# Performance work log

Measured on AMD Instinct MI355X. Metric: run time of the kernel, lower is better.

## Reference

```python
import jax, jax.numpy as jnp
import numpy as np

TAU = 0.5

def setup_inputs() -> dict:
    key = jax.random.key(0)
    ks = jax.random.split(key, 20)
    B, D1, D2, E1, E2, U = 4096, 2000, 2000, 256, 256, 512
    M = E1 + E2
    s = lambda k, shp, scale=0.05: jax.random.normal(k, shp, dtype=jnp.float32) * scale
    return {
        "inputs": jax.random.normal(ks[0], (B, D1 + D2), dtype=jnp.float32),
        "h_tm1": jax.random.normal(ks[1], (B, U), dtype=jnp.float32),
        "crohis_tm": jax.random.normal(ks[2], (B, M), dtype=jnp.float32),
        "embed_weight_1": s(ks[3], (D1, E1)),
        "embed_weight_2": s(ks[4], (D2, E2)),
        "ca_1to2_w": s(ks[5], (E1, E1)),
        "ca_1to2_u": s(ks[6], (E2, E1)),
        "ca_1to2_v": s(ks[7], (E2, E1)),
        "ca_2to1_w": s(ks[8], (E2, E2)),
        "ca_2to1_u": s(ks[9], (E1, E2)),
        "ca_2to1_v": s(ks[10], (E1, E2)),
        "crohis_weight_w": s(ks[11], (M, U)),
        "crohis_bias": jnp.zeros((U,), jnp.float32),
        "crohis_decomp_weight": s(ks[12], (M, M)),
        "crohis_decomp_bias": jnp.zeros((M,), jnp.float32),
        "kernel": s(ks[13], (M, 3 * U)),
        "recurrent_kernel": s(ks[14], (U, 3 * U)),
        "bias": jnp.zeros((3 * U,), jnp.float32),
    }


def reference(inputs, h_tm1, crohis_tm,
              embed_weight_1, embed_weight_2,
              ca_1to2_w, ca_1to2_u, ca_1to2_v,
              ca_2to1_w, ca_2to1_u, ca_2to1_v,
              crohis_weight_w, crohis_bias,
              crohis_decomp_weight, crohis_decomp_bias,
              kernel, recurrent_kernel, bias):
    D1 = embed_weight_1.shape[0]
    U = recurrent_kernel.shape[0]
    # dual embedding lookups (dense multi-hot x embedding matrix)
    seqx1 = inputs[:, :D1]
    seqx2 = inputs[:, D1:]
    emb1 = seqx1 @ embed_weight_1   # [B, E1]
    emb2 = seqx2 @ embed_weight_2   # [B, E2]
    # cross-attention gates (softmax over feature axis, as K.softmax default)
    att12 = jax.nn.softmax(jnp.tanh(emb1 @ ca_1to2_w + emb2 @ ca_1to2_u) * (emb2 @ ca_1to2_v), axis=-1)
    att21 = jax.nn.softmax(jnp.tanh(emb2 @ ca_2to1_w + emb1 @ ca_2to1_u) * (emb1 @ ca_2to1_v), axis=-1)
    x = jnp.concatenate([emb1 * att12, emb2 * att21], axis=-1)  # [B, M]
    # cross-history decomposition modulating previous hidden state
    cro = jnp.tanh(crohis_tm @ crohis_decomp_weight + crohis_decomp_bias)
    h_prev = h_tm1 + jnp.tanh(cro @ crohis_weight_w + crohis_bias)
    # GRU (implementation=2, reset_after=False)
    mx = x @ kernel + bias                         # [B, 3U]
    x_z, x_r, x_h = mx[:, :U], mx[:, U:2 * U], mx[:, 2 * U:]
    mi = h_prev @ recurrent_kernel[:, :2 * U]      # [B, 2U]
    z = jax.nn.sigmoid(x_z + mi[:, :U])
    r = jax.nn.sigmoid(x_r + mi[:, U:])
    hh = jnp.tanh(x_h + (r * h_prev) @ recurrent_kernel[:, 2 * U:])
    h = z * h_prev + (1.0 - z) * hh
    # updated cross-history state (exponential moving average with tau)
    crohis_new = TAU * crohis_tm + (1.0 - TAU) * x
    return h, crohis_new
```

## Files before the change

kernel.cpp:

```cpp
#include <hip/hip_runtime.h>
#include <hip/hip_bf16.h>
#include <math.h>


#define TAU_F 0.5f

typedef __bf16 bf16x8 __attribute__((ext_vector_type(8)));
typedef __bf16 bf16x4 __attribute__((ext_vector_type(4)));
typedef float f32x4 __attribute__((ext_vector_type(4)));

__device__ __forceinline__ void gload16(const void* g, void* l) {
    __builtin_amdgcn_global_load_lds(
        (const __attribute__((address_space(1))) void*)g,
        (__attribute__((address_space(3))) void*)l, 16, 0, 0);
}

struct SubGemm {
    const void* A;
    int lda;
    int Kvalid;
    const __bf16* BT;
    int ldbt;
    float* C;
    int ldc;
    long long strideC;
    int Ksub;
    int nbx;
    int pairSplit;
    int pairAOff;
    int obf16;
};

template <bool AFP32>
__global__ __launch_bounds__(256) void gemm_dual(SubGemm g1, SubGemm g2, int blocks1)
{
    __shared__ __attribute__((aligned(16))) char lds[49152];

    const int tid = threadIdx.x, w = tid >> 6, l = tid & 63;

    const int gx = gridDim.x;
    const int nwg = gx * (int)gridDim.y;
    const int hw = (int)blockIdx.y * gx + (int)blockIdx.x;
    const int lg = (hw & 7) * (nwg >> 3) + (hw >> 3);
    const int bxl_lin = lg % gx;
    const int by = lg / gx;

    const bool second = bxl_lin >= blocks1;
    const SubGemm& g = second ? g2 : g1;
    const int bxl = second ? bxl_lin - blocks1 : bxl_lin;
    const int ct = bxl % g.nbx, spl = bxl / g.nbx;
    const int brow = by * 64, bcol = ct * 128;
    const int k_begin = spl * g.Ksub;
    const int nt = g.Ksub >> 5;
    const int aoff = (ct >= g.pairSplit) ? g.pairAOff : 0;

    const int sbr = w * 32 + (l >> 2);
    const int seg = (l & 3) * 8;

    const __bf16* Bg0 = g.BT + (size_t)(bcol + sbr) * g.ldbt + seg + k_begin;
    const __bf16* Bg1 = Bg0 + (size_t)16 * g.ldbt;

    f32x4 acc[2][4] = {};
    const int fr = l & 15, fk = (l >> 4) * 8;
    const int wr = (w >> 1) * 32, wc = (w & 1) * 64;
    const int kmax = (nt - 1) * 32;

    if constexpr (AFP32) {
        auto Af32 = (float (*)[64][32])lds;
        auto Bs   = (__bf16 (*)[128][32])(lds + 24576);

        const float* ArowBase = (const float*)g.A + aoff
                              + (size_t)(brow + w * 16 + (l >> 3)) * g.lda;
        const int colLane = (l & 7) * 4;
        const int kcl4 = g.Kvalid - 4;

#define ISSUE_A32(slot)                                                       \
        {                                                                     \
            const int _s = (slot);                                            \
            const int _k = (_s * 32 < kmax) ? _s * 32 : kmax;                 \
            const int _b = _s % 3;                                            \
            int c0 = k_begin + _k + colLane;                                  \
            c0 = c0 < kcl4 ? c0 : kcl4;                                       \
            gload16(ArowBase + c0,                 &Af32[_b][w * 16][0]);     \
            gload16(ArowBase + 8 * g.lda + c0,     &Af32[_b][w * 16 + 8][0]); \
            gload16(Bg0 + _k, &Bs[_b][w * 32][0]);                            \
            gload16(Bg1 + _k, &Bs[_b][w * 32 + 16][0]);                       \
        }

        ISSUE_A32(0) ISSUE_A32(1)

        for (int t = 0; t < nt; ++t) {
            asm volatile("s_waitcnt vmcnt(4)" ::: "memory");
            asm volatile("s_waitcnt lgkmcnt(0)" ::: "memory");
            __builtin_amdgcn_s_barrier();

            const int bi = t % 3;
            bf16x8 a[2]; bf16x8 b[4];
#pragma unroll
            for (int m = 0; m < 2; ++m) {
                f32x4 lo = *(const f32x4*)&Af32[bi][wr + m * 16 + fr][fk];
                f32x4 hi = *(const f32x4*)&Af32[bi][wr + m * 16 + fr][fk + 4];
#pragma unroll
                for (int z = 0; z < 4; ++z) { a[m][z] = (__bf16)lo[z]; a[m][4 + z] = (__bf16)hi[z]; }
            }
#pragma unroll
            for (int n = 0; n < 4; ++n) b[n] = *(const bf16x8*)&Bs[bi][wc + n * 16 + fr][fk];

            ISSUE_A32(t + 2)

#pragma unroll
            for (int m = 0; m < 2; ++m)
#pragma unroll
                for (int n = 0; n < 4; ++n)
                    acc[m][n] = __builtin_amdgcn_mfma_f32_16x16x32_bf16(a[m], b[n], acc[m][n], 0, 0, 0);
        }
#undef ISSUE_A32
    } else {
        auto As = (__bf16 (*)[64][32])lds;
        auto Bs = (__bf16 (*)[128][32])(lds + 16384);

        const int sar = w * 16 + (l >> 2);
        const __bf16* Ar = (const __bf16*)g.A + aoff
                         + (size_t)(brow + sar) * g.lda + seg + k_begin;

#define ISSUE_AB(slot)                                                        \
        {                                                                     \
            const int _s = (slot);                                            \
            const int _k = (_s * 32 < kmax) ? _s * 32 : kmax;                 \
            const int _b = _s & 3;                                            \
            gload16(Ar + _k,  &As[_b][w * 16][0]);                            \
            gload16(Bg0 + _k, &Bs[_b][w * 32][0]);                            \
            gload16(Bg1 + _k, &Bs[_b][w * 32 + 16][0]);                       \
        }

        ISSUE_AB(0) ISSUE_AB(1) ISSUE_AB(2)

        for (int t = 0; t < nt; ++t) {
            asm volatile("s_waitcnt vmcnt(6)" ::: "memory");
            asm volatile("s_waitcnt lgkmcnt(0)" ::: "memory");
            __builtin_amdgcn_s_barrier();

            const int bi = t & 3;
            bf16x8 a[2], b[4];
#pragma unroll
            for (int m = 0; m < 2; ++m) a[m] = *(const bf16x8*)&As[bi][wr + m * 16 + fr][fk];
#pragma unroll
            for (int n = 0; n < 4; ++n) b[n] = *(const bf16x8*)&Bs[bi][wc + n * 16 + fr][fk];

            ISSUE_AB(t + 3)

#pragma unroll
            for (int m = 0; m < 2; ++m)
#pragma unroll
                for (int n = 0; n < 4; ++n)
                    acc[m][n] = __builtin_amdgcn_mfma_f32_16x16x32_bf16(a[m], b[n], acc[m][n], 0, 0, 0);
        }
#undef ISSUE_AB
    }

    const int fq = (l >> 4) * 4;
    if (g.obf16) {
        __bf16* Cb = (__bf16*)g.C + (size_t)spl * g.strideC;
#pragma unroll
        for (int m = 0; m < 2; ++m)
#pragma unroll
            for (int n = 0; n < 4; ++n)
#pragma unroll
                for (int r = 0; r < 4; ++r) {
                    int row = brow + wr + m * 16 + fq + r;
                    int col = bcol + wc + n * 16 + fr;
                    Cb[(size_t)row * g.ldc + col] = (__bf16)acc[m][n][r];
                }
    } else {
        float* C = g.C + (size_t)spl * g.strideC;
#pragma unroll
        for (int m = 0; m < 2; ++m)
#pragma unroll
            for (int n = 0; n < 4; ++n)
#pragma unroll
                for (int r = 0; r < 4; ++r) {
                    int row = brow + wr + m * 16 + fq + r;
                    int col = bcol + wc + n * 16 + fr;
                    C[(size_t)row * g.ldc + col] = acc[m][n][r];
                }
    }
}

__global__ __launch_bounds__(256) void prep_wT(
    const float* __restrict__ ew1, const float* __restrict__ ew2,
    const float* __restrict__ w12, const float* __restrict__ u12,
    const float* __restrict__ v12, const float* __restrict__ w21,
    const float* __restrict__ u21, const float* __restrict__ v21,
    const float* __restrict__ cd_w, const float* __restrict__ cw_w,
    const float* __restrict__ kern, const float* __restrict__ rkern,
    __bf16* __restrict__ WT, __bf16* __restrict__ WcatT,
    __bf16* __restrict__ cdT, __bf16* __restrict__ cwT,
    __bf16* __restrict__ kernT, __bf16* __restrict__ rkernT)
{
    __shared__ float tile[64][65];
    const int b = blockIdx.x, tid = threadIdx.x;
    const int tr = tid >> 6, tc = tid & 63;

    const float* src = nullptr;
    int ldsrc = 0, srow0 = 0, scol0 = 0, kvalid = 1 << 30;
    __bf16* dst; int ldd, n0, k0;
    bool zero = false;

    if (b < 256) {
        int q = b; n0 = (q >> 5) * 64; k0 = (q & 31) * 64;
        dst = WT; ldd = 2048; kvalid = 2000; ldsrc = 256; srow0 = k0;
        if (n0 < 256) { src = ew1; scol0 = n0; } else { src = ew2; scol0 = n0 - 256; }
    } else if (b < 384) {
        int q = b - 256; n0 = (q >> 3) * 64; k0 = (q & 7) * 64;
        dst = WcatT; ldd = 512; ldsrc = 256; srow0 = k0 & 255; scol0 = n0 & 255;
        int qn = n0 >> 8; bool khi = k0 >= 256;
        if (qn == 0)      src = khi ? u12 : w12;
        else if (qn == 1) src = khi ? w21 : u21;
        else if (qn == 2) { if (khi) src = v12; else zero = true; }
        else              { if (khi) zero = true; else src = v21; }
    } else if (b < 448) {
        int q = b - 384; n0 = (q >> 3) * 64; k0 = (q & 7) * 64;
        src = cd_w; ldsrc = 512; srow0 = k0; scol0 = n0; dst = cdT; ldd = 512;
    } else if (b < 512) {
        int q = b - 448; n0 = (q >> 3) * 64; k0 = (q & 7) * 64;
        src = cw_w; ldsrc = 512; srow0 = k0; scol0 = n0; dst = cwT; ldd = 512;
    } else if (b < 704) {
        int q = b - 512; n0 = (q >> 3) * 64; k0 = (q & 7) * 64;
        src = kern; ldsrc = 1536; srow0 = k0; scol0 = n0; dst = kernT; ldd = 512;
    } else {
        int q = b - 704; n0 = (q >> 3) * 64; k0 = (q & 7) * 64;
        src = rkern; ldsrc = 1536; srow0 = k0; scol0 = n0; dst = rkernT; ldd = 512;
    }

#pragma unroll
    for (int p = 0; p < 16; ++p) {
        int kr = p * 4 + tr;
        float v = 0.f;
        if (!zero && (srow0 + kr) < kvalid)
            v = src[(size_t)(srow0 + kr) * ldsrc + scol0 + tc];
        tile[kr][tc] = v;
    }
    __syncthreads();
#pragma unroll
    for (int p = 0; p < 16; ++p) {
        int nr = p * 4 + tr;
        dst[(size_t)(n0 + nr) * ldd + k0 + tc] = (__bf16)tile[tc][nr];
    }
}

__global__ __launch_bounds__(256) void reduce_A(
    const float* __restrict__ P12, const float* __restrict__ P4,
    const float* __restrict__ cd_b,
    __bf16* __restrict__ E, __bf16* __restrict__ cro)
{
    const int S = 1 << 21;
    int b = blockIdx.x;
    int i = (((b & 2047) * 256) + threadIdx.x) * 4;
    if (b < 2048) {
        f32x4 p0 = *(const f32x4*)(P12 + i);
        f32x4 p1 = *(const f32x4*)(P12 + S + i);
        __bf16 o[4];
#pragma unroll
        for (int j = 0; j < 4; ++j) o[j] = (__bf16)(p0[j] + p1[j]);
        *(bf16x4*)&E[i] = *(bf16x4*)o;
    } else {
        f32x4 p0 = *(const f32x4*)(P4 + i);
        int c = i & 511;
        __bf16 o[4];
#pragma unroll
        for (int j = 0; j < 4; ++j) o[j] = (__bf16)tanhf(p0[j] + cd_b[c + j]);
        *(bf16x4*)&cro[i] = *(bf16x4*)o;
    }
}

__global__ __launch_bounds__(256) void fuse1(
    const __bf16* __restrict__ T, const __bf16* __restrict__ E,
    const float* __restrict__ crohis,
    const float* __restrict__ P5,
    const float* __restrict__ h_tm1, const float* __restrict__ cw_b,
    __bf16* __restrict__ x, float* __restrict__ cro_out,
    float* __restrict__ hprev, __bf16* __restrict__ hprev_bf)
{
    __shared__ float s4[4];
    int b = blockIdx.x;
    int j = threadIdx.x;
    if (b < 4096) {
        const __bf16* t = T + (size_t)b * 1024;
        float s12 = tanhf((float)t[j])       * (float)t[512 + j];
        float s21 = tanhf((float)t[256 + j]) * (float)t[768 + j];
        float v = s12;
#pragma unroll
        for (int o = 32; o >= 1; o >>= 1) v = fmaxf(v, __shfl_xor(v, o, 64));
        __syncthreads(); if ((j & 63) == 0) s4[j >> 6] = v; __syncthreads();
        float m12 = fmaxf(fmaxf(s4[0], s4[1]), fmaxf(s4[2], s4[3]));
        float e12 = expf(s12 - m12);
        v = e12;
#pragma unroll
        for (int o = 32; o >= 1; o >>= 1) v += __shfl_xor(v, o, 64);
        __syncthreads(); if ((j & 63) == 0) s4[j >> 6] = v; __syncthreads();
        float sum12 = s4[0] + s4[1] + s4[2] + s4[3];
        v = s21;
#pragma unroll
        for (int o = 32; o >= 1; o >>= 1) v = fmaxf(v, __shfl_xor(v, o, 64));
        __syncthreads(); if ((j & 63) == 0) s4[j >> 6] = v; __syncthreads();
        float m21 = fmaxf(fmaxf(s4[0], s4[1]), fmaxf(s4[2], s4[3]));
        float e21 = expf(s21 - m21);
        v = e21;
#pragma unroll
        for (int o = 32; o >= 1; o >>= 1) v += __shfl_xor(v, o, 64);
        __syncthreads(); if ((j & 63) == 0) s4[j >> 6] = v; __syncthreads();
        float sum21 = s4[0] + s4[1] + s4[2] + s4[3];

        size_t b0 = (size_t)b * 512 + j, b1 = b0 + 256;
        float x1 = (float)E[b0] * (e12 / sum12);
        float x2 = (float)E[b1] * (e21 / sum21);
        x[b0] = (__bf16)x1;
        x[b1] = (__bf16)x2;
        cro_out[b0] = TAU_F * crohis[b0] + (1.f - TAU_F) * x1;
        cro_out[b1] = TAU_F * crohis[b1] + (1.f - TAU_F) * x2;
    } else {
        int i = ((b - 4096) * 256 + j) * 4;
        f32x4 p = *(const f32x4*)(P5 + i);
        f32x4 ht = *(const f32x4*)(h_tm1 + i);
        int c = i & 511;
        f32x4 o; __bf16 ob[4];
#pragma unroll
        for (int q = 0; q < 4; ++q) {
            float hv = ht[q] + tanhf(p[q] + cw_b[c + q]);
            o[q] = hv; ob[q] = (__bf16)hv;
        }
        *(f32x4*)(hprev + i) = o;
        *(bf16x4*)&hprev_bf[i] = *(bf16x4*)ob;
    }
}

__global__ __launch_bounds__(256) void gates_k(
    const float* __restrict__ mx, const float* __restrict__ mi2,
    const float* __restrict__ hprev, const float* __restrict__ bias,
    __bf16* __restrict__ rh)
{
    int i = (blockIdx.x * 256 + threadIdx.x) * 4;
    int row = i >> 9, c = i & 511;
    f32x4 a  = *(const f32x4*)(mx + (size_t)row * 1536 + 512 + c);
    f32x4 m  = *(const f32x4*)(mi2 + (size_t)row * 1024 + 512 + c);
    f32x4 hp = *(const f32x4*)(hprev + i);
    f32x4 bb = *(const f32x4*)(bias + 512 + c);
    __bf16 o[4];
#pragma unroll
    for (int q = 0; q < 4; ++q) {
        float r = 1.f / (1.f + expf(-(a[q] + bb[q] + m[q])));
        o[q] = (__bf16)(r * hp[q]);
    }
    *(bf16x4*)&rh[i] = *(bf16x4*)o;
}

__global__ __launch_bounds__(256) void final_k(
    const float* __restrict__ mx, const float* __restrict__ mi2,
    const float* __restrict__ P8a, const float* __restrict__ P8b,
    const float* __restrict__ hprev, const float* __restrict__ bias,
    float* __restrict__ h)
{
    int i = (blockIdx.x * 256 + threadIdx.x) * 4;
    int row = i >> 9, c = i & 511;
    f32x4 xz = *(const f32x4*)(mx + (size_t)row * 1536 + c);
    f32x4 xh = *(const f32x4*)(mx + (size_t)row * 1536 + 1024 + c);
    f32x4 mz = *(const f32x4*)(mi2 + (size_t)row * 1024 + c);
    f32x4 p0 = *(const f32x4*)(P8a + i);
    f32x4 p1 = *(const f32x4*)(P8b + i);
    f32x4 hp = *(const f32x4*)(hprev + i);
    f32x4 bz = *(const f32x4*)(bias + c);
    f32x4 bh = *(const f32x4*)(bias + 1024 + c);
    f32x4 o;
#pragma unroll
    for (int q = 0; q < 4; ++q) {
        float z = 1.f / (1.f + expf(-(xz[q] + bz[q] + mz[q])));
        float hh = tanhf(xh[q] + bh[q] + p0[q] + p1[q]);
        o[q] = z * hp[q] + (1.f - z) * hh;
    }
    *(f32x4*)(h + i) = o;
}

extern "C" void kernel_launch(void* const* d_in, const int* in_sizes, int n_in,
                              void* d_out, int out_size, void* d_ws, size_t ws_size,
                              hipStream_t stream)
{
    (void)in_sizes; (void)n_in; (void)out_size; (void)ws_size;

    const float* inputs = (const float*)d_in[0];
    const float* h_tm1  = (const float*)d_in[1];
    const float* crohis = (const float*)d_in[2];
    const float* ew1    = (const float*)d_in[3];
    const float* ew2    = (const float*)d_in[4];
    const float* ca12w  = (const float*)d_in[5];
    const float* ca12u  = (const float*)d_in[6];
    const float* ca12v  = (const float*)d_in[7];
    const float* ca21w  = (const float*)d_in[8];
    const float* ca21u  = (const float*)d_in[9];
    const float* ca21v  = (const float*)d_in[10];
    const float* cw_w   = (const float*)d_in[11];
    const float* cw_b   = (const float*)d_in[12];
    const float* cd_w   = (const float*)d_in[13];
    const float* cd_b   = (const float*)d_in[14];
    const float* kern   = (const float*)d_in[15];
    const float* rkern  = (const float*)d_in[16];
    const float* bias   = (const float*)d_in[17];

    char* ws = (char*)d_ws;
    const size_t MB = 1 << 20;
    float*  P12      = (float*)(ws + 0);
    float*  P4       = (float*)(ws + 16 * MB);
    __bf16* T        = (__bf16*)(ws + 16 * MB);
    float*  P5       = (float*)(ws + 32 * MB);
    __bf16* x        = (__bf16*)(ws + 40 * MB);
    __bf16* rh       = (__bf16*)(ws + 40 * MB);
    float*  P8       = (float*)(ws + 44 * MB);
    __bf16* E        = (__bf16*)(ws + 48 * MB);
    __bf16* cro_bf   = (__bf16*)(ws + 52 * MB);
    float*  hprev    = (float*)(ws + 60 * MB);
    __bf16* hprev_bf = (__bf16*)(ws + 68 * MB);
    float*  mx       = (float*)(ws + 0);
    float*  mi2      = (float*)(ws + 24 * MB);
    __bf16* WT       = (__bf16*)(ws + 72 * MB);
    __bf16* WcatT    = (__bf16*)(ws + 74 * MB);
    __bf16* cdT      = (__bf16*)(ws + 75 * MB);
    __bf16* cwT      = (__bf16*)(ws + 75 * MB + 512 * 1024);
    __bf16* kernT    = (__bf16*)(ws + 76 * MB);
    __bf16* rkernT   = (__bf16*)(ws + 77 * MB + 512 * 1024);

    float* h_out   = (float*)d_out;
    float* cro_out = (float*)d_out + 2 * 1048576;

    const int BIG = 1 << 30;
    const long long S2 = 1ll << 21;

    prep_wT<<<896, 256, 0, stream>>>(ew1, ew2, ca12w, ca12u, ca12v, ca21w,
                                     ca21u, ca21v, cd_w, cw_w, kern, rkern,
                                     WT, WcatT, cdT, cwT, kernT, rkernT);

    SubGemm gA1 = { inputs, 4000, 2000, WT,  2048, P12, 512, S2, 1024, 4, 2, 2000, 0 };
    SubGemm gA2 = { crohis,  512,  512, cdT,  512, P4,  512, 0,   512, 4, BIG, 0, 0 };
    gemm_dual<true><<<dim3(12, 64), 256, 0, stream>>>(gA1, gA2, 8);

    reduce_A<<<4096, 256, 0, stream>>>(P12, P4, cd_b, E, cro_bf);

    SubGemm gB1 = { E,      512, 512, WcatT, 512, (float*)T, 1024, 0, 512, 8, BIG, 0, 1 };
    SubGemm gB2 = { cro_bf, 512, 512, cwT,   512, P5,        512,  0, 512, 4, BIG, 0, 0 };
    gemm_dual<false><<<dim3(12, 64), 256, 0, stream>>>(gB1, gB2, 8);

    fuse1<<<6144, 256, 0, stream>>>(T, E, crohis, P5, h_tm1, cw_b,
                                    x, cro_out, hprev, hprev_bf);

    SubGemm gC1 = { x,        512, 512, kernT,  512, mx,  1536, 0, 512, 12, BIG, 0, 0 };
    SubGemm gC2 = { hprev_bf, 512, 512, rkernT, 512, mi2, 1024, 0, 512, 8,  BIG, 0, 0 };
    gemm_dual<false><<<dim3(20, 64), 256, 0, stream>>>(gC1, gC2, 12);

    gates_k<<<2048, 256, 0, stream>>>(mx, mi2, hprev, bias, rh);

    SubGemm gG = { rh, 512, 512, rkernT + (size_t)1024 * 512, 512, P8, 512, S2, 256, 4, BIG, 0, 0 };
    gemm_dual<false><<<dim3(8, 64), 256, 0, stream>>>(gG, gG, 8);

    final_k<<<2048, 256, 0, stream>>>(mx, mi2, P8, P8 + S2, hprev, bias, h_out);
}
```

Before: 132.7 us.

## Drop multi-stage LDS pipelining and raise split-K for more workgroups

The GEMM kernel gives up its 3/4-stage global_load_lds ring buffer for a single-buffered load/sync/compute loop, cutting LDS per workgroup from 48KB to 12-16KB so more workgroups fit per CU. Split-K is raised for the embedding GEMM (4-way) and for the crohis decomposition and crohis-weight GEMMs (2-way), which increases grid sizes. The reduce and fuse kernels now sum the extra partials, and workspace buffers are reassigned so the additional partial outputs fit. The cost is that load latency is no longer hidden inside a workgroup, and the extra partials add memory traffic.

```diff
diff --git a/kernel.cpp b/kernel.cpp
--- a/kernel.cpp
+++ b/kernel.cpp
@@ -34,7 +34,7 @@
 template <bool AFP32>
 __global__ __launch_bounds__(256) void gemm_dual(SubGemm g1, SubGemm g2, int blocks1)
 {
-    __shared__ __attribute__((aligned(16))) char lds[49152];
+    __shared__ __attribute__((aligned(16))) char lds[AFP32 ? 16384 : 12288];
 
     const int tid = threadIdx.x, w = tid >> 6, l = tid & 63;
 
@@ -63,99 +63,71 @@
     f32x4 acc[2][4] = {};
     const int fr = l & 15, fk = (l >> 4) * 8;
     const int wr = (w >> 1) * 32, wc = (w & 1) * 64;
-    const int kmax = (nt - 1) * 32;
 
     if constexpr (AFP32) {
-        auto Af32 = (float (*)[64][32])lds;
-        auto Bs   = (__bf16 (*)[128][32])(lds + 24576);
-
-        const float* ArowBase = (const float*)g.A + aoff
-                              + (size_t)(brow + w * 16 + (l >> 3)) * g.lda;
+        auto As32 = (float (*)[32])lds;
+        auto Bs   = (__bf16 (*)[32])(lds + 8192);
+
+        const float* Ar0 = (const float*)g.A + aoff
+                         + (size_t)(brow + w * 16 + (l >> 3)) * g.lda;
+        const float* Ar8 = Ar0 + (size_t)8 * g.lda;
         const int colLane = (l & 7) * 4;
         const int kcl4 = g.Kvalid - 4;
 
-#define ISSUE_A32(slot)                                                       \
-        {                                                                     \
-            const int _s = (slot);                                            \
-            const int _k = (_s * 32 < kmax) ? _s * 32 : kmax;                 \
-            const int _b = _s % 3;                                            \
-            int c0 = k_begin + _k + colLane;                                  \
-            c0 = c0 < kcl4 ? c0 : kcl4;                                       \
-            gload16(ArowBase + c0,                 &Af32[_b][w * 16][0]);     \
-            gload16(ArowBase + 8 * g.lda + c0,     &Af32[_b][w * 16 + 8][0]); \
-            gload16(Bg0 + _k, &Bs[_b][w * 32][0]);                            \
-            gload16(Bg1 + _k, &Bs[_b][w * 32 + 16][0]);                       \
-        }
-
-        ISSUE_A32(0) ISSUE_A32(1)
-
         for (int t = 0; t < nt; ++t) {
-            asm volatile("s_waitcnt vmcnt(4)" ::: "memory");
-            asm volatile("s_waitcnt lgkmcnt(0)" ::: "memory");
-            __builtin_amdgcn_s_barrier();
-
-            const int bi = t % 3;
-            bf16x8 a[2]; bf16x8 b[4];
+            const int k = t * 32;
+            __syncthreads();
+            int c0 = k_begin + k + colLane;
+            c0 = c0 < kcl4 ? c0 : kcl4;
+            gload16(Ar0 + c0, &As32[w * 16][0]);
+            gload16(Ar8 + c0, &As32[w * 16 + 8][0]);
+            gload16(Bg0 + k,  &Bs[w * 32][0]);
+            gload16(Bg1 + k,  &Bs[w * 32 + 16][0]);
+            __syncthreads();
+
+            bf16x8 a[2], b[4];
 #pragma unroll
             for (int m = 0; m < 2; ++m) {
-                f32x4 lo = *(const f32x4*)&Af32[bi][wr + m * 16 + fr][fk];
-                f32x4 hi = *(const f32x4*)&Af32[bi][wr + m * 16 + fr][fk + 4];
+                f32x4 lo = *(const f32x4*)&As32[wr + m * 16 + fr][fk];
+                f32x4 hi = *(const f32x4*)&As32[wr + m * 16 + fr][fk + 4];
 #pragma unroll
                 for (int z = 0; z < 4; ++z) { a[m][z] = (__bf16)lo[z]; a[m][4 + z] = (__bf16)hi[z]; }
             }
 #pragma unroll
-            for (int n = 0; n < 4; ++n) b[n] = *(const bf16x8*)&Bs[bi][wc + n * 16 + fr][fk];
-
-            ISSUE_A32(t + 2)
-
+            for (int n = 0; n < 4; ++n) b[n] = *(const bf16x8*)&Bs[wc + n * 16 + fr][fk];
 #pragma unroll
             for (int m = 0; m < 2; ++m)
 #pragma unroll
                 for (int n = 0; n < 4; ++n)
                     acc[m][n] = __builtin_amdgcn_mfma_f32_16x16x32_bf16(a[m], b[n], acc[m][n], 0, 0, 0);
         }
-#undef ISSUE_A32
     } else {
-        auto As = (__bf16 (*)[64][32])lds;
-        auto Bs = (__bf16 (*)[128][32])(lds + 16384);
+        auto As = (__bf16 (*)[32])lds;
+        auto Bs = (__bf16 (*)[32])(lds + 4096);
 
         const int sar = w * 16 + (l >> 2);
         const __bf16* Ar = (const __bf16*)g.A + aoff
                          + (size_t)(brow + sar) * g.lda + seg + k_begin;
 
-#define ISSUE_AB(slot)                                                        \
-        {                                                                     \
-            const int _s = (slot);                                            \
-            const int _k = (_s * 32 < kmax) ? _s * 32 : kmax;                 \
-            const int _b = _s & 3;                                            \
-            gload16(Ar + _k,  &As[_b][w * 16][0]);                            \
-            gload16(Bg0 + _k, &Bs[_b][w * 32][0]);                            \
-            gload16(Bg1 + _k, &Bs[_b][w * 32 + 16][0]);                       \
-        }
-
-        ISSUE_AB(0) ISSUE_AB(1) ISSUE_AB(2)
-
         for (int t = 0; t < nt; ++t) {
-            asm volatile("s_waitcnt vmcnt(6)" ::: "memory");
-            asm volatile("s_waitcnt lgkmcnt(0)" ::: "memory");
-            __builtin_amdgcn_s_barrier();
-
-            const int bi = t & 3;
+            const int k = t * 32;
+            __syncthreads();
+            gload16(Ar + k,  &As[w * 16][0]);
+            gload16(Bg0 + k, &Bs[w * 32][0]);
+            gload16(Bg1 + k, &Bs[w * 32 + 16][0]);
+            __syncthreads();
+
             bf16x8 a[2], b[4];
 #pragma unroll
-            for (int m = 0; m < 2; ++m) a[m] = *(const bf16x8*)&As[bi][wr + m * 16 + fr][fk];
-#pragma unroll
-            for (int n = 0; n < 4; ++n) b[n] = *(const bf16x8*)&Bs[bi][wc + n * 16 + fr][fk];
-
-            ISSUE_AB(t + 3)
-
+            for (int m = 0; m < 2; ++m) a[m] = *(const bf16x8*)&As[wr + m * 16 + fr][fk];
+#pragma unroll
+            for (int n = 0; n < 4; ++n) b[n] = *(const bf16x8*)&Bs[wc + n * 16 + fr][fk];
 #pragma unroll
             for (int m = 0; m < 2; ++m)
 #pragma unroll
                 for (int n = 0; n < 4; ++n)
                     acc[m][n] = __builtin_amdgcn_mfma_f32_16x16x32_bf16(a[m], b[n], acc[m][n], 0, 0, 0);
         }
-#undef ISSUE_AB
     }
 
     const int fq = (l >> 4) * 4;
@@ -259,16 +231,19 @@
     if (b < 2048) {
         f32x4 p0 = *(const f32x4*)(P12 + i);
         f32x4 p1 = *(const f32x4*)(P12 + S + i);
+        f32x4 p2 = *(const f32x4*)(P12 + 2 * S + i);
+        f32x4 p3 = *(const f32x4*)(P12 + 3 * S + i);
         __bf16 o[4];
 #pragma unroll
-        for (int j = 0; j < 4; ++j) o[j] = (__bf16)(p0[j] + p1[j]);
+        for (int j = 0; j < 4; ++j) o[j] = (__bf16)((p0[j] + p1[j]) + (p2[j] + p3[j]));
         *(bf16x4*)&E[i] = *(bf16x4*)o;
     } else {
         f32x4 p0 = *(const f32x4*)(P4 + i);
+        f32x4 p1 = *(const f32x4*)(P4 + S + i);
         int c = i & 511;
         __bf16 o[4];
 #pragma unroll
-        for (int j = 0; j < 4; ++j) o[j] = (__bf16)tanhf(p0[j] + cd_b[c + j]);
+        for (int j = 0; j < 4; ++j) o[j] = (__bf16)tanhf(p0[j] + p1[j] + cd_b[c + j]);
         *(bf16x4*)&cro[i] = *(bf16x4*)o;
     }
 }
@@ -276,7 +251,7 @@
 __global__ __launch_bounds__(256) void fuse1(
     const __bf16* __restrict__ T, const __bf16* __restrict__ E,
     const float* __restrict__ crohis,
-    const float* __restrict__ P5,
+    const float* __restrict__ P5a, const float* __restrict__ P5b,
     const float* __restrict__ h_tm1, const float* __restrict__ cw_b,
     __bf16* __restrict__ x, float* __restrict__ cro_out,
     float* __restrict__ hprev, __bf16* __restrict__ hprev_bf)
@@ -320,13 +295,14 @@
         cro_out[b1] = TAU_F * crohis[b1] + (1.f - TAU_F) * x2;
     } else {
         int i = ((b - 4096) * 256 + j) * 4;
-        f32x4 p = *(const f32x4*)(P5 + i);
+        f32x4 p0 = *(const f32x4*)(P5a + i);
+        f32x4 p1 = *(const f32x4*)(P5b + i);
         f32x4 ht = *(const f32x4*)(h_tm1 + i);
         int c = i & 511;
         f32x4 o; __bf16 ob[4];
 #pragma unroll
         for (int q = 0; q < 4; ++q) {
-            float hv = ht[q] + tanhf(p[q] + cw_b[c + q]);
+            float hv = ht[q] + tanhf(p0[q] + p1[q] + cw_b[c + q]);
             o[q] = hv; ob[q] = (__bf16)hv;
         }
         *(f32x4*)(hprev + i) = o;
@@ -408,18 +384,18 @@
     char* ws = (char*)d_ws;
     const size_t MB = 1 << 20;
     float*  P12      = (float*)(ws + 0);
-    float*  P4       = (float*)(ws + 16 * MB);
-    __bf16* T        = (__bf16*)(ws + 16 * MB);
-    float*  P5       = (float*)(ws + 32 * MB);
-    __bf16* x        = (__bf16*)(ws + 40 * MB);
-    __bf16* rh       = (__bf16*)(ws + 40 * MB);
-    float*  P8       = (float*)(ws + 44 * MB);
+    float*  P5       = (float*)(ws + 0);
+    float*  mi2      = (float*)(ws + 0);
+    __bf16* x        = (__bf16*)(ws + 16 * MB);
+    __bf16* rh       = (__bf16*)(ws + 16 * MB);
+    float*  hprev    = (float*)(ws + 20 * MB);
+    __bf16* hprev_bf = (__bf16*)(ws + 28 * MB);
+    float*  P4       = (float*)(ws + 32 * MB);
+    float*  mx       = (float*)(ws + 32 * MB);
     __bf16* E        = (__bf16*)(ws + 48 * MB);
     __bf16* cro_bf   = (__bf16*)(ws + 52 * MB);
-    float*  hprev    = (float*)(ws + 60 * MB);
-    __bf16* hprev_bf = (__bf16*)(ws + 68 * MB);
-    float*  mx       = (float*)(ws + 0);
-    float*  mi2      = (float*)(ws + 24 * MB);
+    __bf16* T        = (__bf16*)(ws + 56 * MB);
+    float*  P8       = (float*)(ws + 56 * MB);
     __bf16* WT       = (__bf16*)(ws + 72 * MB);
     __bf16* WcatT    = (__bf16*)(ws + 74 * MB);
     __bf16* cdT      = (__bf16*)(ws + 75 * MB);
@@ -437,17 +413,17 @@
                                      ca21u, ca21v, cd_w, cw_w, kern, rkern,
                                      WT, WcatT, cdT, cwT, kernT, rkernT);
 
-    SubGemm gA1 = { inputs, 4000, 2000, WT,  2048, P12, 512, S2, 1024, 4, 2, 2000, 0 };
-    SubGemm gA2 = { crohis,  512,  512, cdT,  512, P4,  512, 0,   512, 4, BIG, 0, 0 };
-    gemm_dual<true><<<dim3(12, 64), 256, 0, stream>>>(gA1, gA2, 8);
+    SubGemm gA1 = { inputs, 4000, 2000, WT,  2048, P12, 512, S2, 512, 4, 2, 2000, 0 };
+    SubGemm gA2 = { crohis,  512,  512, cdT,  512, P4,  512, S2, 256, 4, BIG, 0, 0 };
+    gemm_dual<true><<<dim3(24, 64), 256, 0, stream>>>(gA1, gA2, 16);
 
     reduce_A<<<4096, 256, 0, stream>>>(P12, P4, cd_b, E, cro_bf);
 
-    SubGemm gB1 = { E,      512, 512, WcatT, 512, (float*)T, 1024, 0, 512, 8, BIG, 0, 1 };
-    SubGemm gB2 = { cro_bf, 512, 512, cwT,   512, P5,        512,  0, 512, 4, BIG, 0, 0 };
-    gemm_dual<false><<<dim3(12, 64), 256, 0, stream>>>(gB1, gB2, 8);
-
-    fuse1<<<6144, 256, 0, stream>>>(T, E, crohis, P5, h_tm1, cw_b,
+    SubGemm gB1 = { E,      512, 512, WcatT, 512, (float*)T, 1024, 0,  512, 8, BIG, 0, 1 };
+    SubGemm gB2 = { cro_bf, 512, 512, cwT,   512, P5,        512,  S2, 256, 4, BIG, 0, 0 };
+    gemm_dual<false><<<dim3(16, 64), 256, 0, stream>>>(gB1, gB2, 8);
+
+    fuse1<<<6144, 256, 0, stream>>>(T, E, crohis, P5, P5 + S2, h_tm1, cw_b,
                                     x, cro_out, hprev, hprev_bf);
 
     SubGemm gC1 = { x,        512, 512, kernT,  512, mx,  1536, 0, 512, 12, BIG, 0, 0 };
```

Measured after the change: 143.3 us. 8.0% more time.

## Fuse elementwise epilogues into GEMMs and drop split-K partial buffers

Applied to the files above, without the earlier changes.

Removes split-K from the GEMMs (the big embedding GEMM now runs full K=2048 per block with fewer blocks), so the partial-sum reduction kernels go away. Bias, tanh, h_prev and final GRU update epilogues are fused into the GEMM store via a mode switch, eliminating reduce_A, final_k and half of fuse1. Intermediates mx/mi are stored in bf16 to cut traffic. The cost is fewer blocks on the long-K GEMM (512 vs 768, and 256 blocks for the last GEMM), lower parallelism, and more bf16 rounding of the gate pre-activations.

```diff
diff --git a/kernel.cpp b/kernel.cpp
--- a/kernel.cpp
+++ b/kernel.cpp
@@ -22,13 +22,17 @@
     const __bf16* BT;
     int ldbt;
     float* C;
+    __bf16* Cb;
     int ldc;
-    long long strideC;
     int Ksub;
     int nbx;
     int pairSplit;
     int pairAOff;
-    int obf16;
+    int mode;
+    const float* bias;
+    const float* base;
+    const __bf16* mxp;
+    const __bf16* mip;
 };
 
 template <bool AFP32>
@@ -47,17 +51,15 @@
 
     const bool second = bxl_lin >= blocks1;
     const SubGemm& g = second ? g2 : g1;
-    const int bxl = second ? bxl_lin - blocks1 : bxl_lin;
-    const int ct = bxl % g.nbx, spl = bxl / g.nbx;
+    const int ct = second ? bxl_lin - blocks1 : bxl_lin;
     const int brow = by * 64, bcol = ct * 128;
-    const int k_begin = spl * g.Ksub;
     const int nt = g.Ksub >> 5;
     const int aoff = (ct >= g.pairSplit) ? g.pairAOff : 0;
 
     const int sbr = w * 32 + (l >> 2);
     const int seg = (l & 3) * 8;
 
-    const __bf16* Bg0 = g.BT + (size_t)(bcol + sbr) * g.ldbt + seg + k_begin;
+    const __bf16* Bg0 = g.BT + (size_t)(bcol + sbr) * g.ldbt + seg;
     const __bf16* Bg1 = Bg0 + (size_t)16 * g.ldbt;
 
     f32x4 acc[2][4] = {};
@@ -79,10 +81,10 @@
             const int _s = (slot);                                            \
             const int _k = (_s * 32 < kmax) ? _s * 32 : kmax;                 \
             const int _b = _s % 3;                                            \
-            int c0 = k_begin + _k + colLane;                                  \
+            int c0 = _k + colLane;                                            \
             c0 = c0 < kcl4 ? c0 : kcl4;                                       \
-            gload16(ArowBase + c0,                 &Af32[_b][w * 16][0]);     \
-            gload16(ArowBase + 8 * g.lda + c0,     &Af32[_b][w * 16 + 8][0]); \
+            gload16(ArowBase + c0,             &Af32[_b][w * 16][0]);         \
+            gload16(ArowBase + 8 * g.lda + c0, &Af32[_b][w * 16 + 8][0]);     \
             gload16(Bg0 + _k, &Bs[_b][w * 32][0]);                            \
             gload16(Bg1 + _k, &Bs[_b][w * 32 + 16][0]);                       \
         }
@@ -121,7 +123,7 @@
 
         const int sar = w * 16 + (l >> 2);
         const __bf16* Ar = (const __bf16*)g.A + aoff
-                         + (size_t)(brow + sar) * g.lda + seg + k_begin;
+                         + (size_t)(brow + sar) * g.lda + seg;
 
 #define ISSUE_AB(slot)                                                        \
         {                                                                     \
@@ -159,31 +161,38 @@
     }
 
     const int fq = (l >> 4) * 4;
-    if (g.obf16) {
-        __bf16* Cb = (__bf16*)g.C + (size_t)spl * g.strideC;
-#pragma unroll
-        for (int m = 0; m < 2; ++m)
-#pragma unroll
-            for (int n = 0; n < 4; ++n)
-#pragma unroll
-                for (int r = 0; r < 4; ++r) {
-                    int row = brow + wr + m * 16 + fq + r;
-                    int col = bcol + wc + n * 16 + fr;
-                    Cb[(size_t)row * g.ldc + col] = (__bf16)acc[m][n][r];
+    const int mode = g.mode;
+#pragma unroll
+    for (int m = 0; m < 2; ++m)
+#pragma unroll
+        for (int n = 0; n < 4; ++n)
+#pragma unroll
+            for (int r = 0; r < 4; ++r) {
+                int row = brow + wr + m * 16 + fq + r;
+                int col = bcol + wc + n * 16 + fr;
+                float v = acc[m][n][r];
+                if (mode == 0) {
+                    g.C[(size_t)row * g.ldc + col] = v;
+                } else if (mode == 1) {
+                    g.Cb[(size_t)row * g.ldc + col] = (__bf16)v;
+                } else if (mode == 2) {
+                    g.Cb[(size_t)row * g.ldc + col] = (__bf16)(v + g.bias[col]);
+                } else if (mode == 3) {
+                    g.Cb[(size_t)row * g.ldc + col] = (__bf16)tanhf(v + g.bias[col]);
+                } else if (mode == 4) {
+                    float hv = g.base[(size_t)row * 512 + col] + tanhf(v + g.bias[col]);
+                    g.C[(size_t)row * 512 + col] = hv;
+                    g.Cb[(size_t)row * 512 + col] = (__bf16)hv;
+                } else {
+                    float xz = (float)g.mxp[(size_t)row * 1536 + col];
+                    float xh = (float)g.mxp[(size_t)row * 1536 + 1024 + col];
+                    float mz = (float)g.mip[(size_t)row * 1024 + col];
+                    float hp = g.base[(size_t)row * 512 + col];
+                    float z  = 1.f / (1.f + expf(-(xz + mz)));
+                    float hh = tanhf(xh + v);
+                    g.C[(size_t)row * 512 + col] = z * hp + (1.f - z) * hh;
                 }
-    } else {
-        float* C = g.C + (size_t)spl * g.strideC;
-#pragma unroll
-        for (int m = 0; m < 2; ++m)
-#pragma unroll
-            for (int n = 0; n < 4; ++n)
-#pragma unroll
-                for (int r = 0; r < 4; ++r) {
-                    int row = brow + wr + m * 16 + fq + r;
-                    int col = bcol + wc + n * 16 + fr;
-                    C[(size_t)row * g.ldc + col] = acc[m][n][r];
-                }
-    }
+            }
 }
 
 __global__ __launch_bounds__(256) void prep_wT(
@@ -248,136 +257,65 @@
     }
 }
 
-__global__ __launch_bounds__(256) void reduce_A(
-    const float* __restrict__ P12, const float* __restrict__ P4,
-    const float* __restrict__ cd_b,
-    __bf16* __restrict__ E, __bf16* __restrict__ cro)
-{
-    const int S = 1 << 21;
-    int b = blockIdx.x;
-    int i = (((b & 2047) * 256) + threadIdx.x) * 4;
-    if (b < 2048) {
-        f32x4 p0 = *(const f32x4*)(P12 + i);
-        f32x4 p1 = *(const f32x4*)(P12 + S + i);
-        __bf16 o[4];
-#pragma unroll
-        for (int j = 0; j < 4; ++j) o[j] = (__bf16)(p0[j] + p1[j]);
-        *(bf16x4*)&E[i] = *(bf16x4*)o;
-    } else {
-        f32x4 p0 = *(const f32x4*)(P4 + i);
-        int c = i & 511;
-        __bf16 o[4];
-#pragma unroll
-        for (int j = 0; j < 4; ++j) o[j] = (__bf16)tanhf(p0[j] + cd_b[c + j]);
-        *(bf16x4*)&cro[i] = *(bf16x4*)o;
-    }
-}
-
-__global__ __launch_bounds__(256) void fuse1(
+__global__ __launch_bounds__(256) void fuse_att(
     const __bf16* __restrict__ T, const __bf16* __restrict__ E,
     const float* __restrict__ crohis,
-    const float* __restrict__ P5,
-    const float* __restrict__ h_tm1, const float* __restrict__ cw_b,
-    __bf16* __restrict__ x, float* __restrict__ cro_out,
-    float* __restrict__ hprev, __bf16* __restrict__ hprev_bf)
+    __bf16* __restrict__ x, float* __restrict__ cro_out)
 {
     __shared__ float s4[4];
     int b = blockIdx.x;
     int j = threadIdx.x;
-    if (b < 4096) {
-        const __bf16* t = T + (size_t)b * 1024;
-        float s12 = tanhf((float)t[j])       * (float)t[512 + j];
-        float s21 = tanhf((float)t[256 + j]) * (float)t[768 + j];
-        float v = s12;
-#pragma unroll
-        for (int o = 32; o >= 1; o >>= 1) v = fmaxf(v, __shfl_xor(v, o, 64));
-        __syncthreads(); if ((j & 63) == 0) s4[j >> 6] = v; __syncthreads();
-        float m12 = fmaxf(fmaxf(s4[0], s4[1]), fmaxf(s4[2], s4[3]));
-        float e12 = expf(s12 - m12);
-        v = e12;
-#pragma unroll
-        for (int o = 32; o >= 1; o >>= 1) v += __shfl_xor(v, o, 64);
-        __syncthreads(); if ((j & 63) == 0) s4[j >> 6] = v; __syncthreads();
-        float sum12 = s4[0] + s4[1] + s4[2] + s4[3];
-        v = s21;
-#pragma unroll
-        for (int o = 32; o >= 1; o >>= 1) v = fmaxf(v, __shfl_xor(v, o, 64));
-        __syncthreads(); if ((j & 63) == 0) s4[j >> 6] = v; __syncthreads();
-        float m21 = fmaxf(fmaxf(s4[0], s4[1]), fmaxf(s4[2], s4[3]));
-        float e21 = expf(s21 - m21);
-        v = e21;
-#pragma unroll
-        for (int o = 32; o >= 1; o >>= 1) v += __shfl_xor(v, o, 64);
-        __syncthreads(); if ((j & 63) == 0) s4[j >> 6] = v; __syncthreads();
-        float sum21 = s4[0] + s4[1] + s4[2] + s4[3];
-
-        size_t b0 = (size_t)b * 512 + j, b1 = b0 + 256;
-        float x1 = (float)E[b0] * (e12 / sum12);
-        float x2 = (float)E[b1] * (e21 / sum21);
-        x[b0] = (__bf16)x1;
-        x[b1] = (__bf16)x2;
-        cro_out[b0] = TAU_F * crohis[b0] + (1.f - TAU_F) * x1;
-        cro_out[b1] = TAU_F * crohis[b1] + (1.f - TAU_F) * x2;
-    } else {
-        int i = ((b - 4096) * 256 + j) * 4;
-        f32x4 p = *(const f32x4*)(P5 + i);
-        f32x4 ht = *(const f32x4*)(h_tm1 + i);
-        int c = i & 511;
-        f32x4 o; __bf16 ob[4];
-#pragma unroll
-        for (int q = 0; q < 4; ++q) {
-            float hv = ht[q] + tanhf(p[q] + cw_b[c + q]);
-            o[q] = hv; ob[q] = (__bf16)hv;
-        }
-        *(f32x4*)(hprev + i) = o;
-        *(bf16x4*)&hprev_bf[i] = *(bf16x4*)ob;
-    }
+    const __bf16* t = T + (size_t)b * 1024;
+    float s12 = tanhf((float)t[j])       * (float)t[512 + j];
+    float s21 = tanhf((float)t[256 + j]) * (float)t[768 + j];
+    float v = s12;
+#pragma unroll
+    for (int o = 32; o >= 1; o >>= 1) v = fmaxf(v, __shfl_xor(v, o, 64));
+    __syncthreads(); if ((j & 63) == 0) s4[j >> 6] = v; __syncthreads();
+    float m12 = fmaxf(fmaxf(s4[0], s4[1]), fmaxf(s4[2], s4[3]));
+    float e12 = expf(s12 - m12);
+    v = e12;
+#pragma unroll
+    for (int o = 32; o >= 1; o >>= 1) v += __shfl_xor(v, o, 64);
+    __syncthreads(); if ((j & 63) == 0) s4[j >> 6] = v; __syncthreads();
+    float sum12 = s4[0] + s4[1] + s4[2] + s4[3];
+    v = s21;
+#pragma unroll
+    for (int o = 32; o >= 1; o >>= 1) v = fmaxf(v, __shfl_xor(v, o, 64));
+    __syncthreads(); if ((j & 63) == 0) s4[j >> 6] = v; __syncthreads();
+    float m21 = fmaxf(fmaxf(s4[0], s4[1]), fmaxf(s4[2], s4[3]));
+    float e21 = expf(s21 - m21);
+    v = e21;
+#pragma unroll
+    for (int o = 32; o >= 1; o >>= 1) v += __shfl_xor(v, o, 64);
+    __syncthreads(); if ((j & 63) == 0) s4[j >> 6] = v; __syncthreads();
+    float sum21 = s4[0] + s4[1] + s4[2] + s4[3];
+
+    size_t b0 = (size_t)b * 512 + j, b1 = b0 + 256;
+    float x1 = (float)E[b0] * (e12 / sum12);
+    float x2 = (float)E[b1] * (e21 / sum21);
+    x[b0] = (__bf16)x1;
+    x[b1] = (__bf16)x2;
+    cro_out[b0] = TAU_F * crohis[b0] + (1.f - TAU_F) * x1;
+    cro_out[b1] = TAU_F * crohis[b1] + (1.f - TAU_F) * x2;
 }
 
 __global__ __launch_bounds__(256) void gates_k(
-    const float* __restrict__ mx, const float* __restrict__ mi2,
-    const float* __restrict__ hprev, const float* __restrict__ bias,
-    __bf16* __restrict__ rh)
+    const __bf16* __restrict__ mx, const __bf16* __restrict__ mi,
+    const __bf16* __restrict__ hprev_bf, __bf16* __restrict__ rh)
 {
     int i = (blockIdx.x * 256 + threadIdx.x) * 4;
     int row = i >> 9, c = i & 511;
-    f32x4 a  = *(const f32x4*)(mx + (size_t)row * 1536 + 512 + c);
-    f32x4 m  = *(const f32x4*)(mi2 + (size_t)row * 1024 + 512 + c);
-    f32x4 hp = *(const f32x4*)(hprev + i);
-    f32x4 bb = *(const f32x4*)(bias + 512 + c);
+    bf16x4 a  = *(const bf16x4*)(mx + (size_t)row * 1536 + 512 + c);
+    bf16x4 m  = *(const bf16x4*)(mi + (size_t)row * 1024 + 512 + c);
+    bf16x4 hp = *(const bf16x4*)(hprev_bf + i);
     __bf16 o[4];
 #pragma unroll
     for (int q = 0; q < 4; ++q) {
-        float r = 1.f / (1.f + expf(-(a[q] + bb[q] + m[q])));
-        o[q] = (__bf16)(r * hp[q]);
+        float r = 1.f / (1.f + expf(-((float)a[q] + (float)m[q])));
+        o[q] = (__bf16)(r * (float)hp[q]);
     }
     *(bf16x4*)&rh[i] = *(bf16x4*)o;
-}
-
-__global__ __launch_bounds__(256) void final_k(
-    const float* __restrict__ mx, const float* __restrict__ mi2,
-    const float* __restrict__ P8a, const float* __restrict__ P8b,
-    const float* __restrict__ hprev, const float* __restrict__ bias,
-    float* __restrict__ h)
-{
-    int i = (blockIdx.x * 256 + threadIdx.x) * 4;
-    int row = i >> 9, c = i & 511;
-    f32x4 xz = *(const f32x4*)(mx + (size_t)row * 1536 + c);
-    f32x4 xh = *(const f32x4*)(mx + (size_t)row * 1536 + 1024 + c);
-    f32x4 mz = *(const f32x4*)(mi2 + (size_t)row * 1024 + c);
-    f32x4 p0 = *(const f32x4*)(P8a + i);
-    f32x4 p1 = *(const f32x4*)(P8b + i);
-    f32x4 hp = *(const f32x4*)(hprev + i);
-    f32x4 bz = *(const f32x4*)(bias + c);
-    f32x4 bh = *(const f32x4*)(bias + 1024 + c);
-    f32x4 o;
-#pragma unroll
-    for (int q = 0; q < 4; ++q) {
-        float z = 1.f / (1.f + expf(-(xz[q] + bz[q] + mz[q])));
-        float hh = tanhf(xh[q] + bh[q] + p0[q] + p1[q]);
-        o[q] = z * hp[q] + (1.f - z) * hh;
-    }
-    *(f32x4*)(h + i) = o;
 }
 
 extern "C" void kernel_launch(void* const* d_in, const int* in_sizes, int n_in,
@@ -407,57 +345,47 @@
 
     char* ws = (char*)d_ws;
     const size_t MB = 1 << 20;
-    float*  P12      = (float*)(ws + 0);
-    float*  P4       = (float*)(ws + 16 * MB);
-    __bf16* T        = (__bf16*)(ws + 16 * MB);
-    float*  P5       = (float*)(ws + 32 * MB);
-    __bf16* x        = (__bf16*)(ws + 40 * MB);
-    __bf16* rh       = (__bf16*)(ws + 40 * MB);
-    float*  P8       = (float*)(ws + 44 * MB);
-    __bf16* E        = (__bf16*)(ws + 48 * MB);
-    __bf16* cro_bf   = (__bf16*)(ws + 52 * MB);
-    float*  hprev    = (float*)(ws + 60 * MB);
-    __bf16* hprev_bf = (__bf16*)(ws + 68 * MB);
-    float*  mx       = (float*)(ws + 0);
-    float*  mi2      = (float*)(ws + 24 * MB);
-    __bf16* WT       = (__bf16*)(ws + 72 * MB);
-    __bf16* WcatT    = (__bf16*)(ws + 74 * MB);
-    __bf16* cdT      = (__bf16*)(ws + 75 * MB);
-    __bf16* cwT      = (__bf16*)(ws + 75 * MB + 512 * 1024);
-    __bf16* kernT    = (__bf16*)(ws + 76 * MB);
-    __bf16* rkernT   = (__bf16*)(ws + 77 * MB + 512 * 1024);
+    __bf16* E        = (__bf16*)(ws + 0);
+    __bf16* cro_bf   = (__bf16*)(ws + 4 * MB);
+    __bf16* T        = (__bf16*)(ws + 8 * MB);
+    __bf16* x        = (__bf16*)(ws + 16 * MB);
+    float*  hprev    = (float*)(ws + 20 * MB);
+    __bf16* hprev_bf = (__bf16*)(ws + 36 * MB);
+    __bf16* mx_bf    = (__bf16*)(ws + 40 * MB);
+    __bf16* mi2_bf   = (__bf16*)(ws + 52 * MB);
+    __bf16* rh       = (__bf16*)(ws + 60 * MB);
+    __bf16* WT       = (__bf16*)(ws + 64 * MB);
+    __bf16* WcatT    = (__bf16*)(ws + 66 * MB);
+    __bf16* cdT      = (__bf16*)(ws + 67 * MB);
+    __bf16* cwT      = (__bf16*)(ws + 67 * MB + 512 * 1024);
+    __bf16* kernT    = (__bf16*)(ws + 68 * MB);
+    __bf16* rkernT   = (__bf16*)(ws + 69 * MB + 512 * 1024);
 
     float* h_out   = (float*)d_out;
     float* cro_out = (float*)d_out + 2 * 1048576;
 
     const int BIG = 1 << 30;
-    const long long S2 = 1ll << 21;
 
     prep_wT<<<896, 256, 0, stream>>>(ew1, ew2, ca12w, ca12u, ca12v, ca21w,
                                      ca21u, ca21v, cd_w, cw_w, kern, rkern,
                                      WT, WcatT, cdT, cwT, kernT, rkernT);
 
-    SubGemm gA1 = { inputs, 4000, 2000, WT,  2048, P12, 512, S2, 1024, 4, 2, 2000, 0 };
-    SubGemm gA2 = { crohis,  512,  512, cdT,  512, P4,  512, 0,   512, 4, BIG, 0, 0 };
-    gemm_dual<true><<<dim3(12, 64), 256, 0, stream>>>(gA1, gA2, 8);
-
-    reduce_A<<<4096, 256, 0, stream>>>(P12, P4, cd_b, E, cro_bf);
-
-    SubGemm gB1 = { E,      512, 512, WcatT, 512, (float*)T, 1024, 0, 512, 8, BIG, 0, 1 };
-    SubGemm gB2 = { cro_bf, 512, 512, cwT,   512, P5,        512,  0, 512, 4, BIG, 0, 0 };
+    SubGemm gA1 = { inputs, 4000, 2000, WT,  2048, nullptr, E,      512, 2048, 4, 2,   2000, 1, nullptr, nullptr, nullptr, nullptr };
+    SubGemm gA2 = { crohis,  512,  512, cdT,  512, nullptr, cro_bf, 512,  512, 4, BIG, 0,    3, cd_b,    nullptr, nullptr, nullptr };
+    gemm_dual<true><<<dim3(8, 64), 256, 0, stream>>>(gA1, gA2, 4);
+
+    SubGemm gB1 = { E,      512, 512, WcatT, 512, nullptr, T,        1024, 512, 8, BIG, 0, 1, nullptr, nullptr, nullptr, nullptr };
+    SubGemm gB2 = { cro_bf, 512, 512, cwT,   512, hprev,   hprev_bf, 512,  512, 4, BIG, 0, 4, cw_b,    h_tm1,   nullptr, nullptr };
     gemm_dual<false><<<dim3(12, 64), 256, 0, stream>>>(gB1, gB2, 8);
 
-    fuse1<<<6144, 256, 0, stream>>>(T, E, crohis, P5, h_tm1, cw_b,
-                                    x, cro_out, hprev, hprev_bf);
-
-    SubGemm gC1 = { x,        512, 512, kernT,  512, mx,  1536, 0, 512, 12, BIG, 0, 0 };
-    SubGemm gC2 = { hprev_bf, 512, 512, rkernT, 512, mi2, 1024, 0, 512, 8,  BIG, 0, 0 };
+    fuse_att<<<4096, 256, 0, stream>>>(T, E, crohis, x, cro_out);
+
+    SubGemm gC1 = { x,        512, 512, kernT,  512, nullptr, mx_bf,  1536, 512, 12, BIG, 0, 2, bias,    nullptr, nullptr, nullptr };
+    SubGemm gC2 = { hprev_bf, 512, 512, rkernT, 512, nullptr, mi2_bf, 1024, 512, 8,  BIG, 0, 1, nullptr, nullptr, nullptr, nullptr };
     gemm_dual<false><<<dim3(20, 64), 256, 0, stream>>>(gC1, gC2, 12);
 
-    gates_k<<<2048, 256, 0, stream>>>(mx, mi2, hprev, bias, rh);
-
-    SubGemm gG = { rh, 512, 512, rkernT + (size_t)1024 * 512, 512, P8, 512, S2, 256, 4, BIG, 0, 0 };
-    gemm_dual<false><<<dim3(8, 64), 256, 0, stream>>>(gG, gG, 8);
-
-    final_k<<<2048, 256, 0, stream>>>(mx, mi2, P8, P8 + S2, hprev, bias, h_out);
-}
+    gates_k<<<2048, 256, 0, stream>>>(mx_bf, mi2_bf, hprev_bf, rh);
+
+    SubGemm gG = { rh, 512, 512, rkernT + (size_t)1024 * 512, 512, h_out, nullptr, 512, 512, 4, BIG, 0, 5, nullptr, hprev, mx_bf, mi2_bf };
+    gemm_dual<false><<<dim3(4, 64), 256, 0, stream>>>(gG, gG, 4);
+}
```

Result: slower. 175.0 us (+31.9%).

## Fuse final GRU gate epilogue into the last recurrent GEMM, drop split-K

Applied to the files above, without the earlier changes.

Replaces the split-K (2-way) candidate-hidden GEMM plus a separate elementwise final kernel with one GEMM kernel that runs the full K=512 and computes z, tanh and the hidden-state blend in its epilogue. This removes the fp32 partial-sum round trip through workspace and one kernel launch. In exchange the grid shrinks from 512 to 256 workgroups, and the epilogue does scalar, less coalesced reads of mx, mi2 and hprev, so there is less parallelism on the GPU.

```diff
diff --git a/kernel.cpp b/kernel.cpp
--- a/kernel.cpp
+++ b/kernel.cpp
@@ -184,6 +184,96 @@
                     C[(size_t)row * g.ldc + col] = acc[m][n][r];
                 }
     }
+}
+
+__global__ __launch_bounds__(256) void gemm_g8(
+    const __bf16* __restrict__ A, const __bf16* __restrict__ BT,
+    const float* __restrict__ mx, const float* __restrict__ mi2,
+    const float* __restrict__ hprev, const float* __restrict__ bias,
+    float* __restrict__ h)
+{
+    __shared__ __attribute__((aligned(16))) char lds[49152];
+
+    const int tid = threadIdx.x, w = tid >> 6, l = tid & 63;
+
+    const int gx = gridDim.x;
+    const int nwg = gx * (int)gridDim.y;
+    const int hw = (int)blockIdx.y * gx + (int)blockIdx.x;
+    const int lg = (hw & 7) * (nwg >> 3) + (hw >> 3);
+    const int ct = lg % gx;
+    const int by = lg / gx;
+
+    const int brow = by * 64, bcol = ct * 128;
+    const int nt = 16;
+
+    const int sbr = w * 32 + (l >> 2);
+    const int seg = (l & 3) * 8;
+
+    const __bf16* Bg0 = BT + (size_t)(bcol + sbr) * 512 + seg;
+    const __bf16* Bg1 = Bg0 + (size_t)16 * 512;
+
+    f32x4 acc[2][4] = {};
+    const int fr = l & 15, fk = (l >> 4) * 8;
+    const int wr = (w >> 1) * 32, wc = (w & 1) * 64;
+    const int kmax = (nt - 1) * 32;
+
+    auto As = (__bf16 (*)[64][32])lds;
+    auto Bs = (__bf16 (*)[128][32])(lds + 16384);
+
+    const int sar = w * 16 + (l >> 2);
+    const __bf16* Ar = A + (size_t)(brow + sar) * 512 + seg;
+
+#define ISSUE_G8(slot)                                                        \
+    {                                                                         \
+        const int _s = (slot);                                                \
+        const int _k = (_s * 32 < kmax) ? _s * 32 : kmax;                     \
+        const int _b = _s & 3;                                                \
+        gload16(Ar + _k,  &As[_b][w * 16][0]);                                \
+        gload16(Bg0 + _k, &Bs[_b][w * 32][0]);                                \
+        gload16(Bg1 + _k, &Bs[_b][w * 32 + 16][0]);                           \
+    }
+
+    ISSUE_G8(0) ISSUE_G8(1) ISSUE_G8(2)
+
+    for (int t = 0; t < nt; ++t) {
+        asm volatile("s_waitcnt vmcnt(6)" ::: "memory");
+        asm volatile("s_waitcnt lgkmcnt(0)" ::: "memory");
+        __builtin_amdgcn_s_barrier();
+
+        const int bi = t & 3;
+        bf16x8 a[2], b[4];
+#pragma unroll
+        for (int m = 0; m < 2; ++m) a[m] = *(const bf16x8*)&As[bi][wr + m * 16 + fr][fk];
+#pragma unroll
+        for (int n = 0; n < 4; ++n) b[n] = *(const bf16x8*)&Bs[bi][wc + n * 16 + fr][fk];
+
+        ISSUE_G8(t + 3)
+
+#pragma unroll
+        for (int m = 0; m < 2; ++m)
+#pragma unroll
+            for (int n = 0; n < 4; ++n)
+                acc[m][n] = __builtin_amdgcn_mfma_f32_16x16x32_bf16(a[m], b[n], acc[m][n], 0, 0, 0);
+    }
+#undef ISSUE_G8
+
+    const int fq = (l >> 4) * 4;
+#pragma unroll
+    for (int m = 0; m < 2; ++m)
+#pragma unroll
+        for (int n = 0; n < 4; ++n)
+#pragma unroll
+            for (int r = 0; r < 4; ++r) {
+                int row = brow + wr + m * 16 + fq + r;
+                int col = bcol + wc + n * 16 + fr;
+                float xz = mx[(size_t)row * 1536 + col]        + bias[col];
+                float xh = mx[(size_t)row * 1536 + 1024 + col] + bias[1024 + col];
+                float mz = mi2[(size_t)row * 1024 + col];
+                float hp = hprev[(size_t)row * 512 + col];
+                float z  = 1.f / (1.f + expf(-(xz + mz)));
+                float hh = tanhf(xh + acc[m][n][r]);
+                h[(size_t)row * 512 + col] = z * hp + (1.f - z) * hh;
+            }
 }
 
 __global__ __launch_bounds__(256) void prep_wT(
@@ -354,32 +444,6 @@
     *(bf16x4*)&rh[i] = *(bf16x4*)o;
 }
 
-__global__ __launch_bounds__(256) void final_k(
-    const float* __restrict__ mx, const float* __restrict__ mi2,
-    const float* __restrict__ P8a, const float* __restrict__ P8b,
-    const float* __restrict__ hprev, const float* __restrict__ bias,
-    float* __restrict__ h)
-{
-    int i = (blockIdx.x * 256 + threadIdx.x) * 4;
-    int row = i >> 9, c = i & 511;
-    f32x4 xz = *(const f32x4*)(mx + (size_t)row * 1536 + c);
-    f32x4 xh = *(const f32x4*)(mx + (size_t)row * 1536 + 1024 + c);
-    f32x4 mz = *(const f32x4*)(mi2 + (size_t)row * 1024 + c);
-    f32x4 p0 = *(const f32x4*)(P8a + i);
-    f32x4 p1 = *(const f32x4*)(P8b + i);
-    f32x4 hp = *(const f32x4*)(hprev + i);
-    f32x4 bz = *(const f32x4*)(bias + c);
-    f32x4 bh = *(const f32x4*)(bias + 1024 + c);
-    f32x4 o;
-#pragma unroll
-    for (int q = 0; q < 4; ++q) {
-        float z = 1.f / (1.f + expf(-(xz[q] + bz[q] + mz[q])));
-        float hh = tanhf(xh[q] + bh[q] + p0[q] + p1[q]);
-        o[q] = z * hp[q] + (1.f - z) * hh;
-    }
-    *(f32x4*)(h + i) = o;
-}
-
 extern "C" void kernel_launch(void* const* d_in, const int* in_sizes, int n_in,
                               void* d_out, int out_size, void* d_ws, size_t ws_size,
                               hipStream_t stream)
@@ -413,7 +477,6 @@
     float*  P5       = (float*)(ws + 32 * MB);
     __bf16* x        = (__bf16*)(ws + 40 * MB);
     __bf16* rh       = (__bf16*)(ws + 40 * MB);
-    float*  P8       = (float*)(ws + 44 * MB);
     __bf16* E        = (__bf16*)(ws + 48 * MB);
     __bf16* cro_bf   = (__bf16*)(ws + 52 * MB);
     float*  hprev    = (float*)(ws + 60 * MB);
@@ -456,8 +519,6 @@
 
     gates_k<<<2048, 256, 0, stream>>>(mx, mi2, hprev, bias, rh);
 
-    SubGemm gG = { rh, 512, 512, rkernT + (size_t)1024 * 512, 512, P8, 512, S2, 256, 4, BIG, 0, 0 };
-    gemm_dual<false><<<dim3(8, 64), 256, 0, stream>>>(gG, gG, 8);
-
-    final_k<<<2048, 256, 0, stream>>>(mx, mi2, P8, P8 + S2, hprev, bias, h_out);
-}
+    gemm_g8<<<dim3(4, 64), 256, 0, stream>>>(
+        rh, rkernT + (size_t)1024 * 512, mx, mi2, hprev, bias, h_out);
+}
```

Result: no change. 131.9 us (median of 3 runs) (-0.6%).
